# Kernel tuning notes

Measured on AMD Instinct MI355X. Metric: run time of the kernel, lower is better.

The kernel has to match this reference:

```python
import jax, jax.numpy as jnp
import numpy as np

N = 50000
E = 800000
IN_C = 128
OUT_C = 128
N_TYPES = 3
NEG_SLOPE = 0.2  # PyG GATConv default negative_slope


def setup_inputs() -> dict:
    key = jax.random.key(0)
    ks = jax.random.split(key, 10)
    x = jax.random.normal(ks[0], (N, IN_C), dtype=jnp.float32)
    edge_index = jax.random.randint(ks[1], (2, E), 0, N, dtype=jnp.int32)
    edge_type = jax.random.randint(ks[2], (E,), 0, N_TYPES, dtype=jnp.int32)
    node_type = jax.random.randint(ks[3], (N,), 0, 3, dtype=jnp.int32)
    s = 1.0 / np.sqrt(IN_C)
    emb_table = jax.random.normal(ks[4], (3, IN_C), dtype=jnp.float32)
    W = jax.random.normal(ks[5], (N_TYPES, IN_C, OUT_C), dtype=jnp.float32) * s
    att_src = jax.random.normal(ks[6], (N_TYPES, OUT_C), dtype=jnp.float32) * s
    att_dst = jax.random.normal(ks[7], (N_TYPES, OUT_C), dtype=jnp.float32) * s
    bias = jax.random.normal(ks[8], (N_TYPES, OUT_C), dtype=jnp.float32) * 0.01
    return {"x": x, "edge_index": edge_index, "edge_type": edge_type,
            "node_type": node_type, "emb_table": emb_table, "W": W,
            "att_src": att_src, "att_dst": att_dst, "bias": bias}


def reference(x, edge_index, edge_type, node_type, emb_table, W, att_src, att_dst, bias):
    # Eval mode: dropouts are identity. edge_index is non-empty -> GAT branch.
    n = x.shape[0]
    x = x + emb_table[node_type]  # node-type embedding add
    src, dst = edge_index[0], edge_index[1]
    out_sum = jnp.zeros((n, OUT_C), dtype=x.dtype)
    for t in range(N_TYPES):  # per-edge-type GATConv (heads=1, add_self_loops=True)
        xw = x @ W[t]                       # [N, out]
        a_s = xw @ att_src[t]               # [N] alpha_src per node
        a_d = xw @ att_dst[t]               # [N] alpha_dst per node
        mask = edge_type == t               # [E]
        e_raw = jax.nn.leaky_relu(a_s[src] + a_d[dst], NEG_SLOPE)  # [E]
        e_self = jax.nn.leaky_relu(a_s + a_d, NEG_SLOPE)           # [N] self-loop logit
        e_masked = jnp.where(mask, e_raw, -jnp.inf)
        m = jnp.maximum(jax.ops.segment_max(e_masked, dst, num_segments=n), e_self)
        m = jax.lax.stop_gradient(m)
        w_edge = jnp.where(mask, jnp.exp(e_raw - m[dst]), 0.0)     # [E]
        w_self = jnp.exp(e_self - m)                               # [N]
        denom = jax.ops.segment_sum(w_edge, dst, num_segments=n) + w_self
        num = jax.ops.segment_sum(w_edge[:, None] * xw[src], dst, num_segments=n) \
              + w_self[:, None] * xw
        out_sum = out_sum + num / denom[:, None] + bias[t]
        # (attention weights per type are w_edge/denom[dst]; only node output returned)
    return out_sum
```

## Files before the change

### kernel.cpp

```cpp
#include <hip/hip_runtime.h>
#include <math.h>

#define N_NODES 50000
#define N_EDGES 800000
#define C 128
#define NT 3
#define NEG 0.2f
#define CAP 64

#define GEMM_XB 782

typedef __attribute__((ext_vector_type(8))) short short8;
typedef __attribute__((ext_vector_type(4))) float f32x4;

__device__ __forceinline__ float leaky(float v) { return v > 0.f ? v : NEG * v; }

__device__ __forceinline__ unsigned short f2bf(float f) {
  unsigned int u = __float_as_uint(f);
  u = (u + 0x7FFFu + ((u >> 16) & 1u)) >> 16;
  return (unsigned short)u;
}
__device__ __forceinline__ float bf_lo(unsigned int w) { return __uint_as_float(w << 16); }
__device__ __forceinline__ float bf_hi(unsigned int w) { return __uint_as_float(w & 0xFFFF0000u); }

__global__ void k_prep(const float* __restrict__ W, unsigned short* __restrict__ Wt,
                       int* __restrict__ cnt) {
  int bid = blockIdx.x;
  if (bid < 192) {
    int idx = bid * 256 + threadIdx.x;
    int t = idx >> 14, rem = idx & 16383;
    int n = rem >> 7, k = rem & 127;
    Wt[((size_t)t * C + n) * C + k] = f2bf(W[((size_t)t * C + k) * C + n]);
  } else {
    int i4 = (bid - 192) * 256 + threadIdx.x;
    if (i4 < N_NODES / 4) ((int4*)cnt)[i4] = make_int4(0, 0, 0, 0);
  }
}

__global__ void k_main(const float* __restrict__ x, const int* __restrict__ node_type,
                       const float* __restrict__ emb, const unsigned short* __restrict__ Wt,
                       unsigned short* __restrict__ xwb,
                       const float* __restrict__ att_src, const float* __restrict__ att_dst,
                       float* __restrict__ a_s, float2* __restrict__ ad_es,
                       const int* __restrict__ ei, const int* __restrict__ etype,
                       int* __restrict__ cnt, int* __restrict__ buckets) {
  __shared__ unsigned short As[64][136];
  __shared__ unsigned short Bs[128][136];
  const int bid = blockIdx.x;
  const int tid = threadIdx.x;

  if (bid & 1) {
    int e0 = ((bid >> 1) * 256 + tid) * 4;
    if (e0 + 4 <= N_EDGES) {
      int4 s4 = *(const int4*)(ei + e0);
      int4 d4 = *(const int4*)(ei + N_EDGES + e0);
      int4 t4 = *(const int4*)(etype + e0);
      int p0 = atomicAdd(&cnt[d4.x], 1);
      int p1 = atomicAdd(&cnt[d4.y], 1);
      int p2 = atomicAdd(&cnt[d4.z], 1);
      int p3 = atomicAdd(&cnt[d4.w], 1);
      if (p0 < CAP) buckets[(size_t)d4.x * CAP + p0] = t4.x * N_NODES + s4.x;
      if (p1 < CAP) buckets[(size_t)d4.y * CAP + p1] = t4.y * N_NODES + s4.y;
      if (p2 < CAP) buckets[(size_t)d4.z * CAP + p2] = t4.z * N_NODES + s4.z;
      if (p3 < CAP) buckets[(size_t)d4.w * CAP + p3] = t4.w * N_NODES + s4.w;
    }
    return;
  }

  const int wid = tid >> 6, lane = tid & 63;
  const int m = lane & 15, quad = lane >> 4;
  const int row0 = (bid >> 1) * 64;

#pragma unroll
  for (int it = 0; it < 8; ++it) {
    int c = tid + it * 256;
    int rr = c >> 5, q = c & 31;
    int row = row0 + rr;
    float4 xv = make_float4(0.f, 0.f, 0.f, 0.f);
    int nt = 0;
    if (row < N_NODES) {
      xv = *(const float4*)(x + (size_t)row * C + q * 4);
      nt = node_type[row];
    }
    float4 ev = ((const float4*)emb)[nt * 32 + q];
    ushort4 o;
    o.x = f2bf(xv.x + ev.x); o.y = f2bf(xv.y + ev.y);
    o.z = f2bf(xv.z + ev.z); o.w = f2bf(xv.w + ev.w);
    *(ushort4*)&As[rr][q * 4] = o;
  }
#pragma unroll
  for (int it = 0; it < 8; ++it) {
    int c = tid + it * 256;
    int n = c >> 4, kc = c & 15;
    *(uint4*)&Bs[n][kc * 8] = *(const uint4*)(Wt + (size_t)n * C + kc * 8);
  }
  __syncthreads();

  for (int t = 0; t < NT; ++t) {
    f32x4 acc[8] = {};
#pragma unroll
    for (int k0 = 0; k0 < 128; k0 += 32) {
      short8 a = *(const short8*)&As[wid * 16 + m][k0 + quad * 8];
#pragma unroll
      for (int j = 0; j < 8; ++j) {
        short8 b = *(const short8*)&Bs[j * 16 + m][k0 + quad * 8];
        acc[j] = __builtin_amdgcn_mfma_f32_16x16x32_bf16(a, b, acc[j], 0, 0, 0);
      }
    }

    float ps[4] = {}, pd[4] = {};
#pragma unroll
    for (int j = 0; j < 8; ++j) {
      float as = att_src[t * C + j * 16 + m];
      float ad = att_dst[t * C + j * 16 + m];
#pragma unroll
      for (int reg = 0; reg < 4; ++reg) {
        int row = row0 + wid * 16 + quad * 4 + reg;
        float v = acc[j][reg];
        if (row < N_NODES) xwb[((size_t)t * N_NODES + row) * C + j * 16 + m] = f2bf(v);
        ps[reg] += v * as;
        pd[reg] += v * ad;
      }
    }
#pragma unroll
    for (int off = 1; off < 16; off <<= 1) {
#pragma unroll
      for (int reg = 0; reg < 4; ++reg) {
        ps[reg] += __shfl_xor(ps[reg], off);
        pd[reg] += __shfl_xor(pd[reg], off);
      }
    }
    if (m == 0) {
#pragma unroll
      for (int reg = 0; reg < 4; ++reg) {
        int row = row0 + wid * 16 + quad * 4 + reg;
        if (row < N_NODES) {
          int idx = t * N_NODES + row;
          a_s[idx] = ps[reg];
          ad_es[idx] = make_float2(pd[reg], leaky(ps[reg] + pd[reg]));
        }
      }
    }

    if (t + 1 < NT) {
      __syncthreads();
      const unsigned short* Wtt = Wt + (size_t)(t + 1) * C * C;
#pragma unroll
      for (int it = 0; it < 8; ++it) {
        int c = tid + it * 256;
        int n = c >> 4, kc = c & 15;
        *(uint4*)&Bs[n][kc * 8] = *(const uint4*)(Wtt + (size_t)n * C + kc * 8);
      }
      __syncthreads();
    }
  }
}

__global__ void k_gather(const int* __restrict__ cnt, const int* __restrict__ buckets,
                         const unsigned short* __restrict__ xwb,
                         const float* __restrict__ a_s, const float2* __restrict__ ad_es,
                         const float* __restrict__ bias, float* __restrict__ out) {
  int wid = threadIdx.x >> 6;
  int lane = threadIdx.x & 63;
  int i = blockIdx.x * 4 + wid;
  if (i >= N_NODES) return;
  int n = cnt[i];
  if (n > CAP) n = CAP;

  int idxl = 0;
  if (lane < n) idxl = buckets[(size_t)i * CAP + lane];
  int tl = idxl >= 2 * N_NODES ? 2 : (idxl >= N_NODES ? 1 : 0);
  float as = a_s[idxl];
  float2 am = ad_es[tl * N_NODES + i];
  float wl = (lane < n) ? __expf(leaky(as + am.x) - am.y) : 0.f;

  float s0 = tl == 0 ? wl : 0.f;
  float s1 = tl == 1 ? wl : 0.f;
  float s2 = tl == 2 ? wl : 0.f;
#pragma unroll
  for (int off = 1; off < 64; off <<= 1) {
    s0 += __shfl_xor(s0, off);
    s1 += __shfl_xor(s1, off);
    s2 += __shfl_xor(s2, off);
  }
  float inv3[NT] = {1.f / (s0 + 1.f), 1.f / (s1 + 1.f), 1.f / (s2 + 1.f)};
  float wc = wl * inv3[tl];

  float acc0 = 0.f, acc1 = 0.f;
#pragma unroll
  for (int t = 0; t < NT; ++t) {
    int idx = t * N_NODES + i;
    float coef = inv3[t];
    unsigned int w = ((const unsigned int*)(xwb + (size_t)idx * C))[lane];
    float2 b2 = ((const float2*)(bias + t * C))[lane];
    acc0 += coef * bf_lo(w) + b2.x;
    acc1 += coef * bf_hi(w) + b2.y;
  }

  const unsigned int* xwu = (const unsigned int*)xwb;
  int j = 0;
  for (; j + 16 <= n; j += 16) {
    float ac0 = 0.f, ac1 = 0.f;
#pragma unroll
    for (int k = 0; k < 16; ++k) {
      int idx = __shfl(idxl, j + k);
      float c = __shfl(wc, j + k);
      unsigned int v = xwu[(size_t)idx * (C / 2) + lane];
      ac0 += c * bf_lo(v);
      ac1 += c * bf_hi(v);
    }
    acc0 += ac0; acc1 += ac1;
  }
  for (; j + 8 <= n; j += 8) {
    float ac0 = 0.f, ac1 = 0.f;
#pragma unroll
    for (int k = 0; k < 8; ++k) {
      int idx = __shfl(idxl, j + k);
      float c = __shfl(wc, j + k);
      unsigned int v = xwu[(size_t)idx * (C / 2) + lane];
      ac0 += c * bf_lo(v);
      ac1 += c * bf_hi(v);
    }
    acc0 += ac0; acc1 += ac1;
  }
  for (; j < n; ++j) {
    int idx = __shfl(idxl, j);
    float c = __shfl(wc, j);
    unsigned int v = xwu[(size_t)idx * (C / 2) + lane];
    acc0 += c * bf_lo(v);
    acc1 += c * bf_hi(v);
  }
  ((float2*)(out + (size_t)i * C))[lane] = make_float2(acc0, acc1);
}

extern "C" void kernel_launch(void* const* d_in, const int* in_sizes, int n_in,
                              void* d_out, int out_size, void* d_ws, size_t ws_size,
                              hipStream_t stream) {
  const float* x       = (const float*)d_in[0];
  const int* edge_idx  = (const int*)d_in[1];
  const int* edge_type = (const int*)d_in[2];
  const int* node_type = (const int*)d_in[3];
  const float* emb     = (const float*)d_in[4];
  const float* W       = (const float*)d_in[5];
  const float* att_src = (const float*)d_in[6];
  const float* att_dst = (const float*)d_in[7];
  const float* bias    = (const float*)d_in[8];
  float* out = (float*)d_out;

  unsigned short* xwb = (unsigned short*)d_ws;
  unsigned short* Wt  = xwb + (size_t)NT * N_NODES * C;
  float*  a_s   = (float*)(Wt + (size_t)NT * C * C);
  float2* ad_es = (float2*)(a_s + (size_t)NT * N_NODES);
  int*    cnt   = (int*)(ad_es + (size_t)NT * N_NODES);
  int*    buckets = (int*)(cnt + N_NODES);

  k_prep<<<192 + 49, 256, 0, stream>>>(W, Wt, cnt);

  k_main<<<2 * GEMM_XB, 256, 0, stream>>>(x, node_type, emb, Wt, xwb, att_src, att_dst,
                                          a_s, ad_es, edge_idx, edge_type, cnt, buckets);

  k_gather<<<(N_NODES + 3) / 4, 256, 0, stream>>>(cnt, buckets, xwb, a_s, ad_es, bias, out);
}
```

Before: 189.5 us.

## Use fragment-ordered LDS layout for W, hold A in registers, regroup block interleave

Stores the weight tile in LDS in the order each MFMA lane reads it, so B fragment loads become contiguous 16-byte reads with no bank conflicts. The A fragments are loaded into registers once and the A tile shares the single LDS buffer, which cuts LDS use from two arrays to one and may allow more resident blocks. Block IDs are regrouped so GEMM and edge-bucketing blocks alternate in runs of eight instead of one, and the extra blocks past the limit exit early. The cost is an extra barrier for each type and a few idle blocks.

```diff
diff --git a/kernel.cpp b/kernel.cpp
--- a/kernel.cpp
+++ b/kernel.cpp
@@ -9,6 +9,7 @@
 #define CAP 64
 
 #define GEMM_XB 782
+#define NGROUP 98
 
 typedef __attribute__((ext_vector_type(8))) short short8;
 typedef __attribute__((ext_vector_type(4))) float f32x4;
@@ -44,13 +45,14 @@
                        float* __restrict__ a_s, float2* __restrict__ ad_es,
                        const int* __restrict__ ei, const int* __restrict__ etype,
                        int* __restrict__ cnt, int* __restrict__ buckets) {
-  __shared__ unsigned short As[64][136];
-  __shared__ unsigned short Bs[128][136];
+  __shared__ unsigned short BsL[128 * 128];
   const int bid = blockIdx.x;
   const int tid = threadIdx.x;
-
-  if (bid & 1) {
-    int e0 = ((bid >> 1) * 256 + tid) * 4;
+  const int ord = (bid >> 4) * 8 + (bid & 7);
+  if (ord >= GEMM_XB) return;
+
+  if ((bid >> 3) & 1) {
+    int e0 = (ord * 256 + tid) * 4;
     if (e0 + 4 <= N_EDGES) {
       int4 s4 = *(const int4*)(ei + e0);
       int4 d4 = *(const int4*)(ei + N_EDGES + e0);
@@ -69,8 +71,9 @@
 
   const int wid = tid >> 6, lane = tid & 63;
   const int m = lane & 15, quad = lane >> 4;
-  const int row0 = (bid >> 1) * 64;
-
+  const int row0 = ord * 64;
+
+  unsigned short* As2 = BsL;
 #pragma unroll
   for (int it = 0; it < 8; ++it) {
     int c = tid + it * 256;
@@ -86,24 +89,35 @@
     ushort4 o;
     o.x = f2bf(xv.x + ev.x); o.y = f2bf(xv.y + ev.y);
     o.z = f2bf(xv.z + ev.z); o.w = f2bf(xv.w + ev.w);
-    *(ushort4*)&As[rr][q * 4] = o;
-  }
-#pragma unroll
-  for (int it = 0; it < 8; ++it) {
-    int c = tid + it * 256;
-    int n = c >> 4, kc = c & 15;
-    *(uint4*)&Bs[n][kc * 8] = *(const uint4*)(Wt + (size_t)n * C + kc * 8);
+    *(ushort4*)&As2[rr * 136 + q * 4] = o;
   }
   __syncthreads();
+  short8 afr[4];
+#pragma unroll
+  for (int k0c = 0; k0c < 4; ++k0c)
+    afr[k0c] = *(const short8*)&As2[(wid * 16 + m) * 136 + k0c * 32 + quad * 8];
+  __syncthreads();
 
   for (int t = 0; t < NT; ++t) {
+    const unsigned short* Wtt = Wt + (size_t)t * C * C;
+#pragma unroll
+    for (int it = 0; it < 8; ++it) {
+      int c = tid + it * 256;
+      int n = c & 127, kc = c >> 7;
+      int j = n >> 4, mm = n & 15;
+      int k0c = kc >> 2, q = kc & 3;
+      uint4 v = *(const uint4*)(Wtt + (size_t)n * C + kc * 8);
+      *(uint4*)&BsL[((j * 4 + k0c) * 64 + q * 16 + mm) * 8] = v;
+    }
+    __syncthreads();
+
     f32x4 acc[8] = {};
 #pragma unroll
-    for (int k0 = 0; k0 < 128; k0 += 32) {
-      short8 a = *(const short8*)&As[wid * 16 + m][k0 + quad * 8];
+    for (int k0c = 0; k0c < 4; ++k0c) {
+      short8 a = afr[k0c];
 #pragma unroll
       for (int j = 0; j < 8; ++j) {
-        short8 b = *(const short8*)&Bs[j * 16 + m][k0 + quad * 8];
+        short8 b = *(const short8*)&BsL[((j * 4 + k0c) * 64 + lane) * 8];
         acc[j] = __builtin_amdgcn_mfma_f32_16x16x32_bf16(a, b, acc[j], 0, 0, 0);
       }
     }
@@ -141,18 +155,7 @@
         }
       }
     }
-
-    if (t + 1 < NT) {
-      __syncthreads();
-      const unsigned short* Wtt = Wt + (size_t)(t + 1) * C * C;
-#pragma unroll
-      for (int it = 0; it < 8; ++it) {
-        int c = tid + it * 256;
-        int n = c >> 4, kc = c & 15;
-        *(uint4*)&Bs[n][kc * 8] = *(const uint4*)(Wtt + (size_t)n * C + kc * 8);
-      }
-      __syncthreads();
-    }
+    if (t + 1 < NT) __syncthreads();
   }
 }
 
@@ -256,7 +259,7 @@
 
   k_prep<<<192 + 49, 256, 0, stream>>>(W, Wt, cnt);
 
-  k_main<<<2 * GEMM_XB, 256, 0, stream>>>(x, node_type, emb, Wt, xwb, att_src, att_dst,
+  k_main<<<NGROUP * 16, 256, 0, stream>>>(x, node_type, emb, Wt, xwb, att_src, att_dst,
                                           a_s, ad_es, edge_idx, edge_type, cnt, buckets);
 
   k_gather<<<(N_NODES + 3) / 4, 256, 0, stream>>>(cnt, buckets, xwb, a_s, ad_es, bias, out);
```

Result: slower. 210.5 us (+11.1%).
